# Kernel optimization log

Hardware: AMD Instinct MI355X
Metric: run time of the kernel (lower is better)

The kernel has to match this reference:

```python
import jax, jax.numpy as jnp
import numpy as np

B, N, S, F_IN, H, P, FN, K, NB = 32, 200, 192, 8, 64, 48, 4, 10, 3
EPS = 1e-5


def _layer_norm(x, w, b):
    mu = x.mean(-1, keepdims=True)
    var = ((x - mu) ** 2).mean(-1, keepdims=True)
    return (x - mu) / jnp.sqrt(var + EPS) * w + b


def _forward(x, x_future, adj, node_emb, graph_alpha, in_w, in_b, proj_W, proj_b,
             temp_W, temp_b, gcn_W, gcn_b, ln_w, ln_b, futr_W, futr_b, head_W, head_b):
    # InstanceNorm1d over the time axis S, per (batch*node, feature); affine per feature
    mu = x.mean(axis=2, keepdims=True)
    var = ((x - mu) ** 2).mean(axis=2, keepdims=True)
    x = (x - mu) / jnp.sqrt(var + EPS) * in_w + in_b
    x = x @ proj_W + proj_b                      # [B,N,S,H]
    x = x + node_emb[None, :, None, :]
    # learned adjacency: relu(E E^T), top-k mask per row, softmax over columns
    la = jax.nn.relu(node_emb @ node_emb.T)      # [N,N]
    _, idx = jax.lax.top_k(la, K)
    mask = jnp.zeros_like(la).at[jnp.arange(N)[:, None], idx].set(1.0)
    la = jax.nn.softmax(la * mask, axis=1)
    combined = graph_alpha * adj + (1.0 - graph_alpha) * la
    # DenseGCNConv normalization: set diagonal to 1, symmetric D^-1/2 A D^-1/2
    eye = jnp.eye(N, dtype=x.dtype)
    A = combined * (1.0 - eye) + eye
    d = jnp.maximum(A.sum(-1), 1.0) ** -0.5
    A = d[:, None] * A * d[None, :]
    for i in range(NB):
        # temporal MLP (Linear over time axis) + GELU, residual; dropout is eval-mode identity
        y = jnp.einsum('bnsh,ts->bnth', x, temp_W[i]) + temp_b[i][None, None, :, None]
        x = x + jax.nn.gelu(y, approximate=False)
        # spatial GCN, vectorized over all S timesteps in one einsum
        xw = x @ gcn_W[i]                        # [B,N,S,H]
        g = jnp.einsum('mn,bnsh->bmsh', A, xw) + gcn_b[i]
        x = _layer_norm(x + g, ln_w[i], ln_b[i])
    x_hist = x.reshape(B, N, S * H)
    x_futr = (x_future @ futr_W + futr_b).reshape(B, N, P * H)
    feat = jnp.concatenate([x_hist, x_futr], axis=2)
    return feat @ head_W + head_b                # [B,N,P]


def setup_inputs() -> dict:
    key = jax.random.key(0)
    ks = jax.random.split(key, 10)
    r = lambda k, shp, s=0.05: jax.random.normal(k, shp, jnp.float32) * s
    adj = jax.random.uniform(ks[2], (N, N), jnp.float32)
    adj = adj / adj.sum(axis=1, keepdims=True)
    return {
        'x': jax.random.normal(ks[0], (B, N, S, F_IN), jnp.float32),
        'x_future': jax.random.uniform(ks[1], (B, N, P, FN), jnp.float32),
        'adj': adj,
        'node_emb': r(ks[3], (N, H), 1.0),
        'graph_alpha': jnp.asarray(0.5, jnp.float32),
        'in_w': jnp.ones((F_IN,), jnp.float32),
        'in_b': jnp.zeros((F_IN,), jnp.float32),
        'proj_W': r(ks[4], (F_IN, H)),
        'proj_b': jnp.zeros((H,), jnp.float32),
        'temp_W': r(ks[5], (NB, S, S)),
        'temp_b': jnp.zeros((NB, S), jnp.float32),
        'gcn_W': r(ks[6], (NB, H, H)),
        'gcn_b': jnp.zeros((NB, H), jnp.float32),
        'ln_w': jnp.ones((NB, H), jnp.float32),
        'ln_b': jnp.zeros((NB, H), jnp.float32),
        'futr_W': r(ks[7], (FN, H)),
        'futr_b': jnp.zeros((H,), jnp.float32),
        'head_W': r(ks[8], (S * H + P * H, P)),
        'head_b': jnp.zeros((P,), jnp.float32),
    }


def reference(x, x_future, adj, node_emb, graph_alpha, in_w, in_b, proj_W, proj_b,
              temp_W, temp_b, gcn_W, gcn_b, ln_w, ln_b, futr_W, futr_b, head_W, head_b):
    return _forward(x, x_future, adj, node_emb, graph_alpha, in_w, in_b, proj_W, proj_b,
                    temp_W, temp_b, gcn_W, gcn_b, ln_w, ln_b, futr_W, futr_b, head_W, head_b)
```

## Files before the change

kernel.cpp:

```cpp
#include <hip/hip_runtime.h>
#include <math.h>

#define BB   32
#define NN   200
#define SS   192
#define FIN  8
#define HH   64
#define PP   48
#define FNN  4
#define KK   10
#define NBLK 3
#define EPSF 1e-5f
#define SH   (SS*HH)
#define XSZ  ((size_t)BB*NN*SS*HH)
#define ROWS (BB*NN)

#define XSW   256
#define FSP   72
#define ABFSZ (14*7*512)

typedef __attribute__((ext_vector_type(8))) short bf16x8;
typedef __attribute__((ext_vector_type(4))) float f32x4;
typedef __attribute__((ext_vector_type(16))) float f32x16;

__device__ __forceinline__ float bf2f(unsigned short u) {
    union { unsigned int i; float f; } v; v.i = ((unsigned int)u) << 16; return v.f;
}
__device__ __forceinline__ unsigned short f2bf(float f) {
    union { float f; unsigned int i; } v; v.f = f;
    unsigned int r = v.i + 0x7FFFu + ((v.i >> 16) & 1u);
    return (unsigned short)(r >> 16);
}
__device__ __forceinline__ unsigned int pk2bf(float lo, float hi) {
    return (unsigned int)f2bf(lo) | ((unsigned int)f2bf(hi) << 16);
}

__device__ __forceinline__ float wave_sum(float v) {
    #pragma unroll
    for (int off = 32; off > 0; off >>= 1) v += __shfl_xor(v, off, 64);
    return v;
}
__device__ __forceinline__ float wave_max(float v) {
    #pragma unroll
    for (int off = 32; off > 0; off >>= 1) v = fmaxf(v, __shfl_xor(v, off, 64));
    return v;
}

__global__ void k_adj_row(const float* __restrict__ emb, const float* __restrict__ adj,
                          const float* __restrict__ alpha_p,
                          float* __restrict__ Araw, float* __restrict__ dvec) {
    int r = blockIdx.x;
    int lane = threadIdx.x;
    __shared__ float er[HH];
    __shared__ float la[NN];
    __shared__ float tmp[NN];
    __shared__ float keep[NN];
    er[lane] = emb[r*HH + lane];
    __syncthreads();
    for (int j = lane; j < NN; j += 64) {
        float d = 0.f;
        #pragma unroll 8
        for (int h = 0; h < HH; ++h) d += er[h] * emb[j*HH + h];
        float v = fmaxf(d, 0.f);
        la[j] = v; tmp[j] = v; keep[j] = 0.f;
    }
    __syncthreads();
    for (int it = 0; it < KK; ++it) {
        float bv = -1.f; int bi = NN;
        for (int j = lane; j < NN; j += 64) {
            float v = tmp[j];
            if (v > bv) { bv = v; bi = j; }
        }
        #pragma unroll
        for (int off = 32; off > 0; off >>= 1) {
            float ov = __shfl_xor(bv, off, 64);
            int   oi = __shfl_xor(bi, off, 64);
            if (ov > bv || (ov == bv && oi < bi)) { bv = ov; bi = oi; }
        }
        if (lane == 0) { keep[bi] = 1.f; tmp[bi] = -1.f; }
        __syncthreads();
    }
    float mloc = 0.f;
    for (int j = lane; j < NN; j += 64) {
        float v = (keep[j] > 0.f) ? la[j] : 0.f;
        tmp[j] = v;
        mloc = fmaxf(mloc, v);
    }
    float m = wave_max(mloc);
    float sloc = 0.f;
    for (int j = lane; j < NN; j += 64) sloc += expf(tmp[j] - m);
    float ssum = wave_sum(sloc);
    float alpha = alpha_p[0];
    float rloc = 0.f;
    for (int j = lane; j < NN; j += 64) {
        float soft = expf(tmp[j] - m) / ssum;
        float comb = alpha * adj[r*NN + j] + (1.f - alpha) * soft;
        float a = (j == r) ? 1.f : comb;
        Araw[r*NN + j] = a;
        rloc += a;
    }
    float rs = wave_sum(rloc);
    if (lane == 0) dvec[r] = 1.f / sqrtf(fmaxf(rs, 1.f));
}

__global__ void k_adj_scale(const float* __restrict__ Araw, const float* __restrict__ dvec,
                            float* __restrict__ Amat) {
    int r = blockIdx.x, j = threadIdx.x;
    if (j < NN) Amat[r*NN + j] = Araw[r*NN + j] * dvec[r] * dvec[j];
}

__global__ void k_prep(const float* __restrict__ tW, const float* __restrict__ gW,
                       const float* __restrict__ Amat, unsigned short* __restrict__ tWb,
                       unsigned short* __restrict__ AbF, unsigned short* __restrict__ gWF) {
    int i = blockIdx.x*256 + threadIdx.x;
    if (i < NBLK*SS*SS) tWb[i] = f2bf(tW[i]);
    if (i < ABFSZ) {
        int j = i & 7, l = (i >> 3) & 63;
        int nt = (i >> 9) % 7, ks = i / (7*512);
        int node = nt*32 + (l & 31);
        int k = ks*16 + (l >> 5)*8 + j;
        AbF[i] = (node < NN && k < NN) ? f2bf(Amat[node*NN + k]) : (unsigned short)0;
    }
    if (i < NBLK*4096) {
        int blk = i >> 12, r = i & 4095;
        int j = r & 7, l = (r >> 3) & 63;
        int nt2 = (r >> 9) & 1, ksh = r >> 10;
        int h = ksh*16 + (l >> 5)*8 + j;
        int hp = nt2*32 + (l & 31);
        gWF[i] = f2bf(gW[(blk << 12) + h*HH + hp]);
    }
}

__global__ void k_prep2(const float* __restrict__ hW, const float* __restrict__ fW,
                        const float* __restrict__ fb, const float* __restrict__ hb,
                        unsigned short* __restrict__ hWT, float* __restrict__ C1,
                        float* __restrict__ c0) {
    int i = blockIdx.x*256 + threadIdx.x;
    if (i < PP*SH) {
        int n = i / SH, k = i % SH;
        hWT[i] = f2bf(hW[(size_t)k*PP + n]);
    }
    if (i < PP*FNN*PP) {
        int j = i / PP, p = i % PP;
        int p2 = j >> 2, f = j & 3;
        float s = 0.f;
        #pragma unroll 8
        for (int h = 0; h < HH; ++h)
            s += fW[f*HH + h] * hW[(size_t)(SH + p2*HH + h)*PP + p];
        C1[i] = s;
    }
    if (i < PP) {
        float s = hb[i];
        for (int c = 0; c < PP*HH; ++c)
            s += fb[c & 63] * hW[(size_t)(SH + c)*PP + i];
        c0[i] = s;
    }
}

__device__ __forceinline__ void temporal_mfma_body(const unsigned short* xT,
        unsigned short* __restrict__ xp, const unsigned short* __restrict__ Wb,
        const float* __restrict__ tb, int tid) {
    int lane = tid & 63, w = tid >> 6;
    int col = lane & 15, q = lane >> 4;
    f32x4 acc[3][4];
    #pragma unroll
    for (int tt = 0; tt < 3; ++tt)
        #pragma unroll
        for (int ht = 0; ht < 4; ++ht) acc[tt][ht] = (f32x4){0.f,0.f,0.f,0.f};

    #pragma unroll 2
    for (int k0 = 0; k0 < SS; k0 += 32) {
        bf16x8 a[3], b[4];
        int kc = (k0 >> 3) + q;
        #pragma unroll
        for (int tt = 0; tt < 3; ++tt)
            a[tt] = *(const bf16x8*)(Wb + (size_t)(w*48 + tt*16 + col)*SS + k0 + q*8);
        #pragma unroll
        for (int ht = 0; ht < 4; ++ht) {
            int row = ht*16 + col;
            b[ht] = *(const bf16x8*)(&xT[row*XSW + (((kc ^ ((row>>1)&31)) & 31)<<3)]);
        }
        #pragma unroll
        for (int tt = 0; tt < 3; ++tt)
            #pragma unroll
            for (int ht = 0; ht < 4; ++ht)
                acc[tt][ht] = __builtin_amdgcn_mfma_f32_16x16x32_bf16(a[tt], b[ht], acc[tt][ht], 0, 0, 0);
    }
    #pragma unroll
    for (int tt = 0; tt < 3; ++tt) {
        int t0 = w*48 + tt*16 + q*4;
        float tbv[4];
        #pragma unroll
        for (int r = 0; r < 4; ++r) tbv[r] = tb[t0 + r];
        #pragma unroll
        for (int ht = 0; ht < 4; ++ht) {
            int h = ht*16 + col;
            unsigned long long rr = *(const unsigned long long*)
                (&xT[h*XSW + ((((t0>>3) ^ ((h>>1)&31)) & 31)<<3) + (t0&7)]);
            #pragma unroll
            for (int r = 0; r < 4; ++r) {
                float y = acc[tt][ht][r] + tbv[r];
                float u2 = y * (1.5957691216f + 0.07135481626f*y*y);
                float g = y * __builtin_amdgcn_rcpf(1.f + __expf(-u2));
                xp[(t0 + r)*HH + h] = f2bf(bf2f((unsigned short)(rr >> (16*r))) + g);
            }
        }
    }
}

__global__ __launch_bounds__(256) void k_stage0_temporal(
        const float* __restrict__ x, const float* __restrict__ inw,
        const float* __restrict__ inb, const float* __restrict__ pW,
        const float* __restrict__ pb, const float* __restrict__ emb,
        unsigned short* __restrict__ X, const unsigned short* __restrict__ Wb,
        const float* __restrict__ tb) {
    __shared__ unsigned short xT[HH * XSW];
    float* redf = (float*)xT;
    int bn = blockIdx.x, tid = threadIdx.x;
    int n = bn % NN;
    int lane = tid & 63, w = tid >> 6;
    const float* xin = x + (size_t)bn*SS*FIN;
    int f0 = lane & 7, sl = w*8 + (lane >> 3);
    float xv[6];
    #pragma unroll
    for (int j = 0; j < 6; ++j) xv[j] = xin[(sl*6 + j)*FIN + f0];
    float s1 = 0.f, s2 = 0.f;
    #pragma unroll
    for (int j = 0; j < 6; ++j) { s1 += xv[j]; s2 += xv[j]*xv[j]; }
    #pragma unroll
    for (int off = 8; off <= 32; off <<= 1) {
        s1 += __shfl_xor(s1, off, 64);
        s2 += __shfl_xor(s2, off, 64);
    }
    if (lane < FIN) { redf[w*16 + lane] = s1; redf[w*16 + 8 + lane] = s2; }
    __syncthreads();
    int h = lane;
    float sp8[FIN];
    float cst = pb[h] + emb[n*HH + h];
    #pragma unroll
    for (int f = 0; f < FIN; ++f) {
        float a  = redf[0*16 + f] + redf[1*16 + f] + redf[2*16 + f] + redf[3*16 + f];
        float b2 = redf[0*16+8+f] + redf[1*16+8+f] + redf[2*16+8+f] + redf[3*16+8+f];
        float mu  = a * (1.f/SS);
        float var = b2 * (1.f/SS) - mu*mu;
        float sc  = inw[f] * __builtin_amdgcn_rsqf(var + EPSF);
        float pw  = pW[f*HH + h];
        sp8[f] = sc * pw;
        cst += (inb[f] - mu*sc) * pw;
    }
    __syncthreads();
    const float* xw = xin + (size_t)__builtin_amdgcn_readfirstlane(w * 48 * FIN);
    int key = (h >> 1) & 31;
    for (int j4 = 0; j4 < 12; ++j4) {
        int s0 = w*48 + j4*4;
        unsigned long long pk = 0;
        #pragma unroll
        for (int r = 0; r < 4; ++r) {
            float acc = cst;
            #pragma unroll
            for (int f = 0; f < FIN; ++f) acc += xw[j4*32 + r*FIN + f] * sp8[f];
            pk |= (unsigned long long)f2bf(acc) << (16*r);
        }
        *(unsigned long long*)(&xT[h*XSW + ((((s0>>3) ^ key) & 31)<<3) + (s0&7)]) = pk;
    }
    __syncthreads();
    temporal_mfma_body(xT, X + (size_t)bn*SH, Wb, tb, tid);
}

__global__ __launch_bounds__(256) void k_temporal_mfma(unsigned short* __restrict__ X,
        const unsigned short* __restrict__ Wb, const float* __restrict__ tb) {
    __shared__ unsigned short xT[HH * XSW];
    unsigned int* sm32 = (unsigned int*)xT;
    int bn = blockIdx.x, tid = threadIdx.x;
    unsigned short* xp = X + (size_t)bn*SH;
    const unsigned int* xp32 = (const unsigned int*)xp;
    for (int i = tid; i < 96*32; i += 256) {
        int sp = i >> 5, hp = i & 31;
        unsigned int u0 = xp32[(2*sp)*32 + hp];
        unsigned int u1 = xp32[(2*sp+1)*32 + hp];
        unsigned int lo = (u0 & 0xffffu) | (u1 << 16);
        unsigned int hi = (u0 >> 16) | (u1 & 0xffff0000u);
        int swz = ((((sp>>2) ^ hp) & 31)<<2) + (sp&3);
        sm32[(2*hp)*128 + swz]   = lo;
        sm32[(2*hp+1)*128 + swz] = hi;
    }
    __syncthreads();
    temporal_mfma_body(xT, xp, Wb, tb, tid);
}

__global__ __launch_bounds__(512) void k_spatial_fused(unsigned short* __restrict__ X,
        const unsigned short* __restrict__ AbF, const unsigned short* __restrict__ gWF,
        const float* __restrict__ gb, const float* __restrict__ lnw,
        const float* __restrict__ lnb) {
    __shared__ unsigned short smem[HH * XSW];
    unsigned int* sm32 = (unsigned int*)smem;
    int phys = blockIdx.x;
    int xcd = phys & 7, idx = phys >> 3;
    int b = idx / 24;
    int sp = xcd * 24 + (idx - b * 24);
    int tid = threadIdx.x;
    unsigned short* xbase = X + (size_t)b*NN*SH + sp*HH;
    const unsigned int* xp32 = (const unsigned int*)xbase;

    for (int i = tid; i < 100*32; i += 512) {
        int np = i >> 5, dd = i & 31;
        unsigned int u0 = xp32[(size_t)(2*np)*(SH/2) + dd];
        unsigned int u1 = xp32[(size_t)(2*np+1)*(SH/2) + dd];
        unsigned int lo = (u0 & 0xffffu) | (u1 << 16);
        unsigned int hi = (u0 >> 16) | (u1 & 0xffff0000u);
        int swz = ((((np>>2) ^ dd) & 31)<<2) + (np&3);
        sm32[(2*dd)*128 + swz]   = lo;
        sm32[(2*dd+1)*128 + swz] = hi;
    }
    for (int i = tid; i < 64*12; i += 512) {
        int r = i / 12, kdw = 100 + (i % 12);
        sm32[r*128 + ((((kdw>>2) ^ ((r>>1)&31)) & 31)<<2) + (kdw&3)] = 0;
    }
    __syncthreads();

    int lane = tid & 63, w = tid >> 6;
    int l31 = lane & 31, u = lane >> 5;

    unsigned int Dw[2][8];
    unsigned int Xw[2][8];
    unsigned long long res[2][4];

    if (w < 7) {
        f32x16 acc1[2];
        #pragma unroll
        for (int ht = 0; ht < 2; ++ht)
            #pragma unroll
            for (int e = 0; e < 16; ++e) acc1[ht][e] = 0.f;
        const unsigned short* abp = AbF + (size_t)w*512 + lane*8;
        #pragma unroll
        for (int ks = 0; ks < 14; ++ks) {
            bf16x8 bb = *(const bf16x8*)(abp + (size_t)ks*7*512);
            #pragma unroll
            for (int ht = 0; ht < 2; ++ht) {
                int row = ht*32 + l31;
                int chunk = ks*2 + u;
                bf16x8 a = *(const bf16x8*)(&smem[row*XSW +
                        (((chunk ^ ((row>>1)&31)) & 31)<<3)]);
                acc1[ht] = __builtin_amdgcn_mfma_f32_32x32x16_bf16(a, bb, acc1[ht], 0, 0, 0);
            }
        }
        #pragma unroll
        for (int ht = 0; ht < 2; ++ht)
            #pragma unroll
            for (int k = 0; k < 8; ++k)
                Dw[ht][k] = pk2bf(acc1[ht][2*k], acc1[ht][2*k+1]);
        #pragma unroll
        for (int ht = 0; ht < 2; ++ht)
            #pragma unroll
            for (int k = 0; k < 8; ++k)
                Xw[ht][k] = (unsigned int)__shfl_xor((int)Dw[ht][k], 32, 64);

        #pragma unroll
        for (int nt2 = 0; nt2 < 2; ++nt2) {
            int hp = nt2*32 + l31;
            int key = (hp >> 1) & 31;
            #pragma unroll
            for (int a = 0; a < 4; ++a) {
                int node = w*32 + a*8 + u*4;
                res[nt2][a] = *(const unsigned long long*)
                    (&smem[hp*XSW + ((((node>>3) ^ key) & 31)<<3) + (node&7)]);
            }
        }
    }
    __syncthreads();

    if (w < 7) {
        f32x16 acc2[2];
        #pragma unroll
        for (int nt2 = 0; nt2 < 2; ++nt2)
            #pragma unroll
            for (int e = 0; e < 16; ++e) acc2[nt2][e] = 0.f;
        const unsigned short* gp = gWF + lane*8;
        #pragma unroll
        for (int ht = 0; ht < 2; ++ht)
            #pragma unroll
            for (int s = 0; s < 2; ++s) {
                int ksh = ht*2 + s;
                union { unsigned int w4[4]; bf16x8 v; } a2;
                if (s == 0) {
                    a2.w4[0] = u ? Xw[ht][2] : Dw[ht][0];
                    a2.w4[1] = u ? Xw[ht][3] : Dw[ht][1];
                    a2.w4[2] = u ? Dw[ht][2] : Xw[ht][0];
                    a2.w4[3] = u ? Dw[ht][3] : Xw[ht][1];
                } else {
                    a2.w4[0] = u ? Xw[ht][6] : Dw[ht][4];
                    a2.w4[1] = u ? Xw[ht][7] : Dw[ht][5];
                    a2.w4[2] = u ? Dw[ht][6] : Xw[ht][4];
                    a2.w4[3] = u ? Dw[ht][7] : Xw[ht][5];
                }
                #pragma unroll
                for (int nt2 = 0; nt2 < 2; ++nt2) {
                    bf16x8 bw = *(const bf16x8*)(gp + (size_t)(ksh*2 + nt2)*512);
                    acc2[nt2] = __builtin_amdgcn_mfma_f32_32x32x16_bf16(a2.v, bw, acc2[nt2], 0, 0, 0);
                }
            }

        float gbv[2], lwv[2], lbv[2];
        #pragma unroll
        for (int nt2 = 0; nt2 < 2; ++nt2) {
            int hp = nt2*32 + l31;
            gbv[nt2] = gb[hp]; lwv[nt2] = lnw[hp]; lbv[nt2] = lnb[hp];
        }
        #pragma unroll
        for (int nt2 = 0; nt2 < 2; ++nt2)
            #pragma unroll
            for (int r = 0; r < 16; ++r)
                acc2[nt2][r] += bf2f((unsigned short)(res[nt2][r>>2] >> (16*(r&3)))) + gbv[nt2];
        #pragma unroll
        for (int r = 0; r < 16; ++r) {
            float a0 = acc2[0][r], a1 = acc2[1][r];
            float s1 = a0 + a1, s2 = a0*a0 + a1*a1;
            #pragma unroll
            for (int off = 1; off < 32; off <<= 1) {
                s1 += __shfl_xor(s1, off, 64);
                s2 += __shfl_xor(s2, off, 64);
            }
            float mu  = s1 * (1.f/64.f);
            float var = s2 * (1.f/64.f) - mu*mu;
            float rstd = __builtin_amdgcn_rsqf(var + EPSF);
            int node = w*32 + (r&3) + 8*(r>>2) + 4*u;
            if (node < NN) {
                smem[node*FSP + l31]      = f2bf((a0 - mu)*rstd*lwv[0] + lbv[0]);
                smem[node*FSP + 32 + l31] = f2bf((a1 - mu)*rstd*lwv[1] + lbv[1]);
            }
        }
    }
    __syncthreads();
    for (int i = tid; i < NN*8; i += 512) {
        int node = i >> 3, c16 = i & 7;
        uint4 vv = *(const uint4*)(&smem[node*FSP + c16*8]);
        *(uint4*)(xbase + (size_t)node*SH + c16*8) = vv;
    }
}

__global__ __launch_bounds__(192) void k_head_futr(const float* __restrict__ xfut,
        const float* __restrict__ C1, const float* __restrict__ c0,
        float* __restrict__ out) {
    __shared__ float C1l[192*PP];
    __shared__ float xfl[4*192];
    int tid = threadIdx.x;
    int r0 = blockIdx.x * 4;
    for (int i = tid; i < 192*PP; i += 192) C1l[i] = C1[i];
    for (int i = tid; i < 4*192; i += 192) xfl[i] = xfut[(size_t)r0*192 + i];
    __syncthreads();
    int p = tid % PP, rr = tid / PP;
    float acc = c0[p];
    #pragma unroll 8
    for (int j = 0; j < 192; ++j) acc += xfl[rr*192 + j] * C1l[j*PP + p];
    out[(size_t)(r0 + rr)*PP + p] = acc;
}

#define KSL 1536
__global__ __launch_bounds__(256) void k_head_mfma(const unsigned short* __restrict__ X,
        const unsigned short* __restrict__ hWT, float* __restrict__ out) {
    int tid = threadIdx.x;
    int lane = tid & 63, w = tid >> 6;
    int col = lane & 15, q = lane >> 4;
    int m0 = blockIdx.x*64 + w*16;
    int k0 = blockIdx.y*KSL;
    const unsigned short* xp = X + (size_t)(m0 + col)*SH + k0 + q*8;
    const unsigned short* wp = hWT + (size_t)col*SH + k0 + q*8;
    f32x4 acc[3];
    #pragma unroll
    for (int nt = 0; nt < 3; ++nt) acc[nt] = (f32x4){0.f,0.f,0.f,0.f};
    #pragma unroll 4
    for (int kk = 0; kk < KSL; kk += 32) {
        bf16x8 a = *(const bf16x8*)(xp + kk);
        #pragma unroll
        for (int nt = 0; nt < 3; ++nt) {
            bf16x8 b = *(const bf16x8*)(wp + (size_t)nt*16*SH + kk);
            acc[nt] = __builtin_amdgcn_mfma_f32_16x16x32_bf16(a, b, acc[nt], 0, 0, 0);
        }
    }
    int orow = m0 + q*4;
    #pragma unroll
    for (int nt = 0; nt < 3; ++nt)
        #pragma unroll
        for (int r = 0; r < 4; ++r)
            atomicAdd(&out[(size_t)(orow + r)*PP + nt*16 + col], acc[nt][r]);
}

extern "C" void kernel_launch(void* const* d_in, const int* in_sizes, int n_in,
                              void* d_out, int out_size, void* d_ws, size_t ws_size,
                              hipStream_t stream) {
    const float* x     = (const float*)d_in[0];
    const float* xfut  = (const float*)d_in[1];
    const float* adj   = (const float*)d_in[2];
    const float* emb   = (const float*)d_in[3];
    const float* alpha = (const float*)d_in[4];
    const float* inw   = (const float*)d_in[5];
    const float* inb   = (const float*)d_in[6];
    const float* pW    = (const float*)d_in[7];
    const float* pb    = (const float*)d_in[8];
    const float* tW    = (const float*)d_in[9];
    const float* tb    = (const float*)d_in[10];
    const float* gW    = (const float*)d_in[11];
    const float* gb    = (const float*)d_in[12];
    const float* lnw   = (const float*)d_in[13];
    const float* lnb   = (const float*)d_in[14];
    const float* fW    = (const float*)d_in[15];
    const float* fb    = (const float*)d_in[16];
    const float* hW    = (const float*)d_in[17];
    const float* hb    = (const float*)d_in[18];
    float* out = (float*)d_out;

    unsigned short* bufX = (unsigned short*)d_ws;
    float* Amat = (float*)(bufX + XSZ);
    float* Araw = Amat + NN*NN;
    float* dvec = Araw + NN*NN;
    unsigned short* tWb = (unsigned short*)(dvec + NN);
    unsigned short* AbF = tWb + NBLK*SS*SS;
    unsigned short* gWF = AbF + ABFSZ;
    unsigned short* hWT = gWF + NBLK*HH*HH;
    float* C1 = (float*)(hWT + (size_t)PP*SH);
    float* c0 = C1 + 192*PP;

    k_adj_row<<<NN, 64, 0, stream>>>(emb, adj, alpha, Araw, dvec);
    k_adj_scale<<<NN, 256, 0, stream>>>(Araw, dvec, Amat);
    k_prep<<<(NBLK*SS*SS + 255)/256, 256, 0, stream>>>(tW, gW, Amat, tWb, AbF, gWF);
    k_prep2<<<((size_t)PP*SH + 255)/256, 256, 0, stream>>>(hW, fW, fb, hb, hWT, C1, c0);

    k_stage0_temporal<<<ROWS, 256, 0, stream>>>(x, inw, inb, pW, pb, emb, bufX, tWb, tb);
    k_spatial_fused<<<dim3(SS*BB), 512, 0, stream>>>(bufX, AbF, gWF, gb, lnw, lnb);
    for (int i = 1; i < NBLK; ++i) {
        k_temporal_mfma<<<ROWS, 256, 0, stream>>>(bufX, tWb + (size_t)i*SS*SS, tb + i*SS);
        k_spatial_fused<<<dim3(SS*BB), 512, 0, stream>>>(bufX, AbF, gWF + (size_t)i*HH*HH,
                                                         gb + i*HH, lnw + i*HH, lnb + i*HH);
    }
    k_head_futr<<<ROWS/4, 192, 0, stream>>>(xfut, C1, c0, out);
    k_head_mfma<<<dim3(ROWS/64, 8), 256, 0, stream>>>(bufX, hWT, out);
}
```

Baseline: 1.029 ms.

## Transpose second GCN MFMA so LayerNorm reduces per lane instead of shuffles

Swaps the operands of the second spatial MFMA so each lane holds all 32 hidden features of one node per tile. LayerNorm statistics can then be accumulated mostly in registers, needing one cross-half shuffle instead of a five-step butterfly per row. Bias and LayerNorm parameters are pre-permuted in the prep kernel into the accumulator order so they load as float4 vectors. The residual read from shared memory moves after the second GEMM, and the output staging stride shrinks. The cost is scalar LDS residual loads with a new access pattern, which may hit bank conflicts.

```diff
diff --git a/kernel.cpp b/kernel.cpp
--- a/kernel.cpp
+++ b/kernel.cpp
@@ -16,7 +16,7 @@
 #define ROWS (BB*NN)
 
 #define XSW   256
-#define FSP   72
+#define FSP   68
 #define ABFSZ (14*7*512)
 
 typedef __attribute__((ext_vector_type(8))) short bf16x8;
@@ -110,8 +110,12 @@
 }
 
 __global__ void k_prep(const float* __restrict__ tW, const float* __restrict__ gW,
-                       const float* __restrict__ Amat, unsigned short* __restrict__ tWb,
-                       unsigned short* __restrict__ AbF, unsigned short* __restrict__ gWF) {
+                       const float* __restrict__ Amat, const float* __restrict__ gb,
+                       const float* __restrict__ lnw, const float* __restrict__ lnb,
+                       unsigned short* __restrict__ tWb,
+                       unsigned short* __restrict__ AbF, unsigned short* __restrict__ gWF,
+                       float* __restrict__ gbF, float* __restrict__ lnwF,
+                       float* __restrict__ lnbF) {
     int i = blockIdx.x*256 + threadIdx.x;
     if (i < NBLK*SS*SS) tWb[i] = f2bf(tW[i]);
     if (i < ABFSZ) {
@@ -128,6 +132,13 @@
         int h = ksh*16 + (l >> 5)*8 + j;
         int hp = nt2*32 + (l & 31);
         gWF[i] = f2bf(gW[(blk << 12) + h*HH + hp]);
+    }
+    if (i < NBLK*64) {
+        int blk = i >> 6, u = (i >> 5) & 1, mt = (i >> 4) & 1, r = i & 15;
+        int hp = 32*mt + (r & 3) + 8*(r >> 2) + 4*u;
+        gbF[i]  = gb[blk*HH + hp];
+        lnwF[i] = lnw[blk*HH + hp];
+        lnbF[i] = lnb[blk*HH + hp];
     }
 }
 
@@ -290,8 +301,8 @@
 
 __global__ __launch_bounds__(512) void k_spatial_fused(unsigned short* __restrict__ X,
         const unsigned short* __restrict__ AbF, const unsigned short* __restrict__ gWF,
-        const float* __restrict__ gb, const float* __restrict__ lnw,
-        const float* __restrict__ lnb) {
+        const float* __restrict__ gbF, const float* __restrict__ lnwF,
+        const float* __restrict__ lnbF) {
     __shared__ unsigned short smem[HH * XSW];
     unsigned int* sm32 = (unsigned int*)smem;
     int phys = blockIdx.x;
@@ -320,10 +331,10 @@
 
     int lane = tid & 63, w = tid >> 6;
     int l31 = lane & 31, u = lane >> 5;
-
-    unsigned int Dw[2][8];
-    unsigned int Xw[2][8];
-    unsigned long long res[2][4];
+    int nd = w*32 + l31;
+
+    f32x16 acc2[2];
+    float mu = 0.f, rstd = 0.f;
 
     if (w < 7) {
         f32x16 acc1[2];
@@ -344,6 +355,7 @@
                 acc1[ht] = __builtin_amdgcn_mfma_f32_32x32x16_bf16(a, bb, acc1[ht], 0, 0, 0);
             }
         }
+        unsigned int Dw[2][8], Xw[2][8];
         #pragma unroll
         for (int ht = 0; ht < 2; ++ht)
             #pragma unroll
@@ -356,25 +368,9 @@
                 Xw[ht][k] = (unsigned int)__shfl_xor((int)Dw[ht][k], 32, 64);
 
         #pragma unroll
-        for (int nt2 = 0; nt2 < 2; ++nt2) {
-            int hp = nt2*32 + l31;
-            int key = (hp >> 1) & 31;
-            #pragma unroll
-            for (int a = 0; a < 4; ++a) {
-                int node = w*32 + a*8 + u*4;
-                res[nt2][a] = *(const unsigned long long*)
-                    (&smem[hp*XSW + ((((node>>3) ^ key) & 31)<<3) + (node&7)]);
-            }
-        }
-    }
-    __syncthreads();
-
-    if (w < 7) {
-        f32x16 acc2[2];
-        #pragma unroll
-        for (int nt2 = 0; nt2 < 2; ++nt2)
-            #pragma unroll
-            for (int e = 0; e < 16; ++e) acc2[nt2][e] = 0.f;
+        for (int mt = 0; mt < 2; ++mt)
+            #pragma unroll
+            for (int e = 0; e < 16; ++e) acc2[mt][e] = 0.f;
         const unsigned short* gp = gWF + lane*8;
         #pragma unroll
         for (int ht = 0; ht < 2; ++ht)
@@ -394,41 +390,58 @@
                     a2.w4[3] = u ? Dw[ht][7] : Xw[ht][5];
                 }
                 #pragma unroll
-                for (int nt2 = 0; nt2 < 2; ++nt2) {
-                    bf16x8 bw = *(const bf16x8*)(gp + (size_t)(ksh*2 + nt2)*512);
-                    acc2[nt2] = __builtin_amdgcn_mfma_f32_32x32x16_bf16(a2.v, bw, acc2[nt2], 0, 0, 0);
+                for (int mt = 0; mt < 2; ++mt) {
+                    bf16x8 bw = *(const bf16x8*)(gp + (size_t)(ksh*2 + mt)*512);
+                    acc2[mt] = __builtin_amdgcn_mfma_f32_32x32x16_bf16(bw, a2.v, acc2[mt], 0, 0, 0);
                 }
             }
 
-        float gbv[2], lwv[2], lbv[2];
-        #pragma unroll
-        for (int nt2 = 0; nt2 < 2; ++nt2) {
-            int hp = nt2*32 + l31;
-            gbv[nt2] = gb[hp]; lwv[nt2] = lnw[hp]; lbv[nt2] = lnb[hp];
-        }
-        #pragma unroll
-        for (int nt2 = 0; nt2 < 2; ++nt2)
-            #pragma unroll
-            for (int r = 0; r < 16; ++r)
-                acc2[nt2][r] += bf2f((unsigned short)(res[nt2][r>>2] >> (16*(r&3)))) + gbv[nt2];
-        #pragma unroll
-        for (int r = 0; r < 16; ++r) {
-            float a0 = acc2[0][r], a1 = acc2[1][r];
-            float s1 = a0 + a1, s2 = a0*a0 + a1*a1;
-            #pragma unroll
-            for (int off = 1; off < 32; off <<= 1) {
-                s1 += __shfl_xor(s1, off, 64);
-                s2 += __shfl_xor(s2, off, 64);
+        const f32x4* gb4 = (const f32x4*)(gbF + u*32);
+        #pragma unroll
+        for (int mt = 0; mt < 2; ++mt)
+            #pragma unroll
+            for (int rq = 0; rq < 4; ++rq) {
+                f32x4 g = gb4[mt*4 + rq];
+                #pragma unroll
+                for (int j = 0; j < 4; ++j) {
+                    int hp = 32*mt + 8*rq + 4*u + j;
+                    unsigned short xr = smem[hp*XSW +
+                        ((((nd>>3) ^ ((hp>>1)&31)) & 31)<<3) + (nd&7)];
+                    acc2[mt][rq*4 + j] += bf2f(xr) + g[j];
+                }
             }
-            float mu  = s1 * (1.f/64.f);
-            float var = s2 * (1.f/64.f) - mu*mu;
-            float rstd = __builtin_amdgcn_rsqf(var + EPSF);
-            int node = w*32 + (r&3) + 8*(r>>2) + 4*u;
-            if (node < NN) {
-                smem[node*FSP + l31]      = f2bf((a0 - mu)*rstd*lwv[0] + lbv[0]);
-                smem[node*FSP + 32 + l31] = f2bf((a1 - mu)*rstd*lwv[1] + lbv[1]);
+        float s1 = 0.f, s2 = 0.f;
+        #pragma unroll
+        for (int mt = 0; mt < 2; ++mt)
+            #pragma unroll
+            for (int r = 0; r < 16; ++r) {
+                float v = acc2[mt][r];
+                s1 += v; s2 += v*v;
             }
-        }
+        s1 += __shfl_xor(s1, 32, 64);
+        s2 += __shfl_xor(s2, 32, 64);
+        mu = s1 * (1.f/64.f);
+        float var = s2 * (1.f/64.f) - mu*mu;
+        rstd = __builtin_amdgcn_rsqf(var + EPSF);
+    }
+    __syncthreads();
+
+    if (w < 7 && nd < NN) {
+        const f32x4* lw4 = (const f32x4*)(lnwF + u*32);
+        const f32x4* lb4 = (const f32x4*)(lnbF + u*32);
+        #pragma unroll
+        for (int mt = 0; mt < 2; ++mt)
+            #pragma unroll
+            for (int rq = 0; rq < 4; ++rq) {
+                f32x4 lw = lw4[mt*4 + rq], lb = lb4[mt*4 + rq];
+                unsigned long long pk = 0;
+                #pragma unroll
+                for (int j = 0; j < 4; ++j) {
+                    float o = (acc2[mt][rq*4 + j] - mu) * rstd * lw[j] + lb[j];
+                    pk |= (unsigned long long)f2bf(o) << (16*j);
+                }
+                *(unsigned long long*)(&smem[nd*FSP + 32*mt + 8*rq + 4*u]) = pk;
+            }
     }
     __syncthreads();
     for (int i = tid; i < NN*8; i += 512) {
@@ -519,18 +532,22 @@
     unsigned short* hWT = gWF + NBLK*HH*HH;
     float* C1 = (float*)(hWT + (size_t)PP*SH);
     float* c0 = C1 + 192*PP;
+    float* gbF  = c0 + PP;
+    float* lnwF = gbF + NBLK*64;
+    float* lnbF = lnwF + NBLK*64;
 
     k_adj_row<<<NN, 64, 0, stream>>>(emb, adj, alpha, Araw, dvec);
     k_adj_scale<<<NN, 256, 0, stream>>>(Araw, dvec, Amat);
-    k_prep<<<(NBLK*SS*SS + 255)/256, 256, 0, stream>>>(tW, gW, Amat, tWb, AbF, gWF);
+    k_prep<<<(NBLK*SS*SS + 255)/256, 256, 0, stream>>>(tW, gW, Amat, gb, lnw, lnb,
+                                                       tWb, AbF, gWF, gbF, lnwF, lnbF);
     k_prep2<<<((size_t)PP*SH + 255)/256, 256, 0, stream>>>(hW, fW, fb, hb, hWT, C1, c0);
 
     k_stage0_temporal<<<ROWS, 256, 0, stream>>>(x, inw, inb, pW, pb, emb, bufX, tWb, tb);
-    k_spatial_fused<<<dim3(SS*BB), 512, 0, stream>>>(bufX, AbF, gWF, gb, lnw, lnb);
+    k_spatial_fused<<<dim3(SS*BB), 512, 0, stream>>>(bufX, AbF, gWF, gbF, lnwF, lnbF);
     for (int i = 1; i < NBLK; ++i) {
         k_temporal_mfma<<<ROWS, 256, 0, stream>>>(bufX, tWb + (size_t)i*SS*SS, tb + i*SS);
         k_spatial_fused<<<dim3(SS*BB), 512, 0, stream>>>(bufX, AbF, gWF + (size_t)i*HH*HH,
-                                                         gb + i*HH, lnw + i*HH, lnb + i*HH);
+                                                         gbF + i*64, lnwF + i*64, lnbF + i*64);
     }
     k_head_futr<<<ROWS/4, 192, 0, stream>>>(xfut, C1, c0, out);
     k_head_mfma<<<dim3(ROWS/64, 8), 256, 0, stream>>>(bufX, hWT, out);
```

After: 952.8 us. -7.4%, faster.
